# Performance work log

Measured on AMD Instinct MI355X. Metric: run time of the kernel, lower is better.

## Reference

```python
import jax, jax.numpy as jnp
import numpy as np

B, T, H, DK, DV, HID, C = 2, 4096, 16, 128, 128, 2048, 64  # chunk size 64 (fla default)
EPS = 1e-5


def setup_inputs() -> dict:
    key = jax.random.key(0)
    ks = jax.random.split(key, 8)
    s = 0.02
    return dict(
        hidden_ab=jax.random.normal(ks[0], (B, T, HID), jnp.float32),
        hidden_g=jax.random.normal(ks[1], (B, T, HID), jnp.float32),
        q=jax.random.normal(ks[2], (B, T, H, DK), jnp.float32),
        k=jax.random.normal(ks[3], (B, T, H, DK), jnp.float32),
        v=jax.random.normal(ks[4], (B, T, H, DV), jnp.float32),
        Wb=jax.random.normal(ks[5], (HID, H), jnp.float32) * s,
        Wg=jax.random.normal(ks[6], (HID, H), jnp.float32) * s,
        o_norm_w=jnp.ones((DV,), jnp.float32),
        o_proj_w=jax.random.normal(ks[7], (H, DV, DK), jnp.float32) * s,
    )


def _l2norm(x):
    return x * jax.lax.rsqrt(jnp.sum(x * x, -1, keepdims=True) + 1e-6)


def reference(hidden_ab, hidden_g, q, k, v, Wb, Wg, o_norm_w, o_proj_w):
    # beta gate per head (training path: sigmoid(b_proj(hidden_ab)))
    beta = jax.nn.sigmoid(hidden_ab @ Wb)  # [B,T,H]
    # qk_norm == 'l2' -> l2 normalization inside the kernel, q scaled by dk^-0.5
    q = _l2norm(q)
    k = _l2norm(k)
    scale = DK ** -0.5
    N = T // C

    def toc(x, d):  # [B,T,H,d] -> [N,B,H,C,d]
        return x.reshape(B, N, C, H, d).transpose(1, 0, 3, 2, 4)

    qc = toc(q * scale, DK)
    kc = toc(k, DK)
    vc = toc(v, DV)
    bc = beta.reshape(B, N, C, H).transpose(1, 0, 3, 2)  # [N,B,H,C]

    k_beta = kc * bc[..., None]
    v_beta = vc * bc[..., None]

    # intra-chunk UT transform: Tm = (I + strict_lower(k_beta k^T))^{-1}
    Lm = jnp.tril(jnp.einsum('nbhik,nbhjk->nbhij', k_beta, kc), -1)  # [N,B,H,C,C]
    eye = jnp.eye(C, dtype=q.dtype)
    Tm = jax.scipy.linalg.solve_triangular(eye + Lm, jnp.broadcast_to(eye, Lm.shape), lower=True)
    u = Tm @ v_beta   # [N,B,H,C,DV]
    w = Tm @ k_beta   # [N,B,H,C,DK]
    attn = jnp.tril(jnp.einsum('nbhik,nbhjk->nbhij', qc, kc))  # causal intra-chunk scores

    def step(S, ins):  # S: [B,H,DK,DV] carried state
        qn, kn, an, un, wn = ins
        vi = un - wn @ S                                   # corrected values
        on = qn @ S + an @ vi                              # inter + intra chunk output
        S = S + jnp.einsum('bhck,bhcv->bhkv', kn, vi)      # state update
        return S, on

    S0 = jnp.zeros((B, H, DK, DV), q.dtype)
    _, o = jax.lax.scan(step, S0, (qc, kc, attn, u, w))    # o: [N,B,H,C,DV]
    o = o.transpose(1, 0, 3, 2, 4).reshape(B, T, H, DV)

    # FusedRMSNormSwishGate with per-head scalar gate broadcast over DV
    g = hidden_g @ Wg  # [B,T,H]
    o = o * jax.lax.rsqrt(jnp.mean(o * o, -1, keepdims=True) + EPS) * o_norm_w
    o = o * (g * jax.nn.sigmoid(g))[..., None]

    # GroupLinear: per-head DV -> head_dim projection, then flatten heads
    out = jnp.einsum('bthv,hvd->bthd', o, o_proj_w).reshape(B, T, H * DK)
    return out
```

## Files before the change

kernel.cpp:

```cpp
#include <hip/hip_runtime.h>
#include <hip/hip_bf16.h>

#define BB 2
#define TT 4096
#define HH 16
#define DKk 128
#define DVv 128
#define HIDD 2048
#define CC 64
#define NN 64
#define GGS 16
#define QSCALE 0.08838834764831845f

static __device__ __forceinline__ unsigned short f2bf(float f) {
  unsigned u = __float_as_uint(f);
  u += 0x7fffu + ((u >> 16) & 1u);
  return (unsigned short)(u >> 16);
}
static __device__ __forceinline__ float bf2f(unsigned short s) {
  return __uint_as_float(((unsigned)s) << 16);
}

static __device__ __forceinline__ void barrier_lds_only() {
  asm volatile("s_waitcnt lgkmcnt(0)\n\ts_barrier" ::: "memory");
}

typedef short bf8 __attribute__((ext_vector_type(8)));
typedef short bf4 __attribute__((ext_vector_type(4)));
typedef float f4 __attribute__((ext_vector_type(4)));

static __device__ __forceinline__ bf4 pack_bf4(float a, float b, float c, float d) {
  bf4 r;
  r[0] = (short)f2bf(a); r[1] = (short)f2bf(b);
  r[2] = (short)f2bf(c); r[3] = (short)f2bf(d);
  return r;
}

__global__ __launch_bounds__(256) void k0_wt(
    const float* __restrict__ Wb, const float* __restrict__ Wg,
    unsigned short* __restrict__ Wtb, unsigned short* __restrict__ Wtg) {
  int blk = blockIdx.x;
  const float* W = (blk < 8) ? Wb : Wg;
  unsigned short* Wt = (blk < 8) ? Wtb : Wtg;
  int k0 = (blk & 7) * 256;
  int tid = threadIdx.x;
  __shared__ unsigned short st[16][272];
  const float* p = W + (size_t)(k0 + tid) * HH;
#pragma unroll
  for (int h4 = 0; h4 < 4; h4++) {
    float4 x = *(const float4*)(p + h4 * 4);
    st[h4 * 4 + 0][tid] = f2bf(x.x);
    st[h4 * 4 + 1][tid] = f2bf(x.y);
    st[h4 * 4 + 2][tid] = f2bf(x.z);
    st[h4 * 4 + 3][tid] = f2bf(x.w);
  }
  __syncthreads();
  int h = tid >> 4, c = (tid & 15) << 4;
#pragma unroll
  for (int j = 0; j < 16; j++)
    Wt[(size_t)h * HIDD + k0 + c + j] = st[h][c + j];
}

__global__ __launch_bounds__(256) void k0p_pt(
    const float* __restrict__ opw, unsigned short* __restrict__ Ppt) {
  int h = blockIdx.x;
  int tid = threadIdx.x;
  __shared__ unsigned short sp[128 * 132];
  const float* P = opw + (size_t)h * (DVv * DKk);
  for (int it = 0; it < 16; it++) {
    int idx = it * 256 + tid;
    int vv = idx >> 5, d4 = (idx & 31) << 2;
    float4 x = *(const float4*)(P + vv * 128 + d4);
    sp[vv * 132 + d4 + 0] = f2bf(x.x);
    sp[vv * 132 + d4 + 1] = f2bf(x.y);
    sp[vv * 132 + d4 + 2] = f2bf(x.z);
    sp[vv * 132 + d4 + 3] = f2bf(x.w);
  }
  __syncthreads();
  unsigned short* dst = Ppt + (size_t)h * (DVv * DKk);
  for (int it = 0; it < 8; it++) {
    int idx = it * 256 + tid;
    int d = idx >> 4, v8 = (idx & 15) << 3;
    unsigned short tmp[8];
#pragma unroll
    for (int j = 0; j < 8; j++) tmp[j] = sp[(v8 + j) * 132 + d];
    *(uint4*)&dst[d * 128 + v8] = *(uint4*)tmp;
  }
}

__global__ __launch_bounds__(256) void k1_beta_g(
    const float* __restrict__ hab, const float* __restrict__ hg,
    const unsigned short* __restrict__ Wtb, const unsigned short* __restrict__ Wtg,
    float* __restrict__ beta, float* __restrict__ graw) {
  int tile = blockIdx.x;
  int tid = threadIdx.x;
  int w = tid >> 6, lane = tid & 63;
  int proj = w >> 1, ks = w & 1;
  int n16 = lane & 15, qd = lane >> 4;
  const float* hid = proj ? hg : hab;
  const unsigned short* Wt = proj ? Wtg : Wtb;
  size_t rowbase = (size_t)(tile * 16 + n16) * HIDD;
  int k0 = ks * 1024;

  f4 acc = {0.f, 0.f, 0.f, 0.f};
  for (int s = 0; s < 32; s++) {
    int kk = k0 + s * 32 + qd * 8;
    const float* hp = hid + rowbase + kk;
    float4 h0 = *(const float4*)hp;
    float4 h1 = *(const float4*)(hp + 4);
    bf8 a;
    a[0] = (short)f2bf(h0.x); a[1] = (short)f2bf(h0.y);
    a[2] = (short)f2bf(h0.z); a[3] = (short)f2bf(h0.w);
    a[4] = (short)f2bf(h1.x); a[5] = (short)f2bf(h1.y);
    a[6] = (short)f2bf(h1.z); a[7] = (short)f2bf(h1.w);
    bf8 b = *(const bf8*)&Wt[(size_t)n16 * HIDD + kk];
    acc = __builtin_amdgcn_mfma_f32_16x16x32_bf16(a, b, acc, 0, 0, 0);
  }

  __shared__ float red[2][16][17];
  if (ks == 1) {
#pragma unroll
    for (int r = 0; r < 4; r++) red[proj][qd * 4 + r][n16] = acc[r];
  }
  __syncthreads();
  if (ks == 0) {
#pragma unroll
    for (int r = 0; r < 4; r++) {
      float s = acc[r] + red[proj][qd * 4 + r][n16];
      size_t t = (size_t)(tile * 16 + qd * 4 + r) * HH + n16;
      if (proj == 0) beta[t] = 1.f / (1.f + expf(-s));
      else           graw[t] = s;
    }
  }
}

__global__ __launch_bounds__(256) void k2_l2norm(
    const float* __restrict__ q, const float* __restrict__ k,
    unsigned short* __restrict__ qn, unsigned short* __restrict__ kn) {
  int lane = threadIdx.x & 63, wave = threadIdx.x >> 6;
  for (int u = 0; u < 2; u++) {
    int vec = blockIdx.x * 8 + wave * 2 + u;
    size_t off = (size_t)vec * 64 + lane;
    float2 q2 = ((const float2*)q)[off];
    float2 k2 = ((const float2*)k)[off];
    float sq = q2.x * q2.x + q2.y * q2.y;
    float sk = k2.x * k2.x + k2.y * k2.y;
#pragma unroll
    for (int m = 32; m; m >>= 1) { sq += __shfl_xor(sq, m); sk += __shfl_xor(sk, m); }
    float rq = rsqrtf(sq + 1e-6f) * QSCALE;
    float rk = rsqrtf(sk + 1e-6f);
    unsigned pq = (unsigned)f2bf(q2.x * rq) | ((unsigned)f2bf(q2.y * rq) << 16);
    unsigned pk = (unsigned)f2bf(k2.x * rk) | ((unsigned)f2bf(k2.y * rk) << 16);
    ((unsigned*)qn)[off] = pq;
    ((unsigned*)kn)[off] = pk;
  }
}

#define SW 72
#define K3_M0R 8704
#define K3_M0T 13312
#define K3_M1R 17920
#define K3_M1T 22528
#define K3_TB  27136
#define K3_ARENA 31744

__global__ __launch_bounds__(256) void k3_chunk(
    const unsigned short* __restrict__ qn, const unsigned short* __restrict__ kn,
    const float* __restrict__ beta,
    unsigned short* __restrict__ ATg, unsigned short* __restrict__ Ktg) {
  int cid = blockIdx.x;
  int n = cid & (NN - 1);
  int bh = cid / NN;
  int h = bh & (HH - 1);
  int b = bh / HH;
  int tid = threadIdx.x;
  int w = tid >> 6;
  int lane = tid & 63;
  int n16 = lane & 15;
  int qd = lane >> 4;
  int r0 = w * 16;

  __shared__ __align__(16) unsigned short arena[K3_ARENA];
  __shared__ float sb[CC];
  unsigned short* sk = arena;
  unsigned short* sq = arena + 8704;

  int t0 = n * CC;
#pragma unroll
  for (int p = 0; p < 4; p++) {
    int id = p * 256 + tid, row = id >> 4, c8 = (id & 15) << 3;
    size_t g = ((size_t)((b * TT + t0 + row) * HH + h)) * DKk + c8;
    *(uint4*)&sk[row * 136 + c8] = *(const uint4*)(kn + g);
    *(uint4*)&sq[row * 136 + c8] = *(const uint4*)(qn + g);
  }
  if (tid < CC) sb[tid] = beta[(size_t)((b * TT + t0 + tid) * HH + h)];
  __syncthreads();

  f4 at[4], mk[4];
#pragma unroll
  for (int ct = 0; ct < 4; ct++) { at[ct] = (f4){0,0,0,0}; mk[ct] = (f4){0,0,0,0}; }
#pragma unroll
  for (int s = 0; s < 4; s++) {
    bf8 aq = *(const bf8*)&sq[(r0 + n16) * 136 + s * 32 + qd * 8];
    bf8 ak = *(const bf8*)&sk[(r0 + n16) * 136 + s * 32 + qd * 8];
#pragma unroll
    for (int ct = 0; ct < 4; ct++) {
      bf8 bk = *(const bf8*)&sk[(ct * 16 + n16) * 136 + s * 32 + qd * 8];
      at[ct] = __builtin_amdgcn_mfma_f32_16x16x32_bf16(aq, bk, at[ct], 0, 0, 0);
      mk[ct] = __builtin_amdgcn_mfma_f32_16x16x32_bf16(ak, bk, mk[ct], 0, 0, 0);
    }
  }

  f4 tf[4];
  float mpv[4][4];
#pragma unroll
  for (int ct = 0; ct < 4; ct++) {
#pragma unroll
    for (int r = 0; r < 4; r++) {
      int i = r0 + qd * 4 + r, j = ct * 16 + n16;
      at[ct][r] = (j <= i) ? at[ct][r] : 0.f;
      float mp = (j < i) ? -sb[i] * mk[ct][r] : 0.f;
      mpv[ct][r] = mp;
      tf[ct][r] = (i == j) ? 1.f : mp;
    }
  }
  __syncthreads();

#pragma unroll
  for (int ct = 0; ct < 4; ct++) {
#pragma unroll
    for (int r = 0; r < 4; r++) {
      int i = r0 + qd * 4 + r, j = ct * 16 + n16;
      unsigned short hm = f2bf(mpv[ct][r]);
      arena[K3_M0R + i * SW + j] = hm;
      arena[K3_M0T + j * SW + i] = hm;
      arena[K3_TB + j * SW + i] = f2bf(tf[ct][r]);
    }
  }
  __syncthreads();

  int p = 0;
  for (int it = 1; it <= 5; it++) {
    int mrp = p ? K3_M1R : K3_M0R, mtp = p ? K3_M1T : K3_M0T;
    int mrn = p ? K3_M0R : K3_M1R, mtn = p ? K3_M0T : K3_M1T;
    f4 nr[4];
#pragma unroll
    for (int ct = 0; ct < 4; ct++) nr[ct] = (f4){0,0,0,0};
#pragma unroll
    for (int s = 0; s < 2; s++) {
      bf8 a = *(const bf8*)&arena[mrp + (r0 + n16) * SW + s * 32 + qd * 8];
#pragma unroll
      for (int ct = 0; ct < 4; ct++) {
        bf8 bb = *(const bf8*)&arena[mtp + (ct * 16 + n16) * SW + s * 32 + qd * 8];
        nr[ct] = __builtin_amdgcn_mfma_f32_16x16x32_bf16(a, bb, nr[ct], 0, 0, 0);
      }
    }
#pragma unroll
    for (int ct = 0; ct < 4; ct++) {
#pragma unroll
      for (int r = 0; r < 4; r++) {
        int i = r0 + qd * 4 + r, j = ct * 16 + n16;
        unsigned short hm = f2bf(nr[ct][r]);
        arena[mrn + i * SW + j] = hm;
        arena[mtn + j * SW + i] = hm;
      }
    }
    __syncthreads();

#pragma unroll
    for (int s = 0; s < 2; s++) {
      bf8 a = *(const bf8*)&arena[mrn + (r0 + n16) * SW + s * 32 + qd * 8];
#pragma unroll
      for (int ct = 0; ct < 4; ct++) {
        bf8 bb = *(const bf8*)&arena[K3_TB + (ct * 16 + n16) * SW + s * 32 + qd * 8];
        tf[ct] = __builtin_amdgcn_mfma_f32_16x16x32_bf16(a, bb, tf[ct], 0, 0, 0);
      }
    }
    __syncthreads();

    if (it < 5) {
#pragma unroll
      for (int ct = 0; ct < 4; ct++) {
#pragma unroll
        for (int r = 0; r < 4; r++) {
          int i = r0 + qd * 4 + r, j = ct * 16 + n16;
          arena[K3_TB + j * SW + i] = f2bf(tf[ct][r]);
        }
      }
    }
    p = 1 - p;
  }

#pragma unroll
  for (int ct = 0; ct < 4; ct++) {
#pragma unroll
    for (int r = 0; r < 4; r++) {
      int i = r0 + qd * 4 + r, j = ct * 16 + n16;
      arena[K3_M0R + i * SW + j] = f2bf(at[ct][r]);
      arena[K3_TB + j * SW + i] = f2bf(tf[ct][r]);
    }
  }
  __syncthreads();

  {
    f4 ac[4];
#pragma unroll
    for (int ct = 0; ct < 4; ct++) ac[ct] = (f4){0,0,0,0};
#pragma unroll
    for (int s = 0; s < 2; s++) {
      bf8 a = *(const bf8*)&arena[K3_M0R + (r0 + n16) * SW + s * 32 + qd * 8];
#pragma unroll
      for (int ct = 0; ct < 4; ct++) {
        bf8 bb = *(const bf8*)&arena[K3_TB + (ct * 16 + n16) * SW + s * 32 + qd * 8];
        ac[ct] = __builtin_amdgcn_mfma_f32_16x16x32_bf16(a, bb, ac[ct], 0, 0, 0);
      }
    }
    size_t abase = (size_t)cid * (CC * CC);
#pragma unroll
    for (int ct = 0; ct < 4; ct++)
#pragma unroll
      for (int r = 0; r < 4; r++)
        ATg[abase + (r0 + qd * 4 + r) * CC + ct * 16 + n16] = f2bf(ac[ct][r]);
  }

  {
    size_t kbase = (size_t)cid * (DKk * CC);
#pragma unroll
    for (int t = 0; t < 2; t++) {
      int dkt = w * 32 + t * 16;
      f4 ac[4];
#pragma unroll
      for (int ct = 0; ct < 4; ct++) ac[ct] = (f4){0,0,0,0};
#pragma unroll
      for (int s = 0; s < 2; s++) {
        bf8 a;
#pragma unroll
        for (int jj = 0; jj < 8; jj++)
          a[jj] = (short)sk[(s * 32 + qd * 8 + jj) * 136 + dkt + n16];
#pragma unroll
        for (int ct = 0; ct < 4; ct++) {
          bf8 bb = *(const bf8*)&arena[K3_TB + (ct * 16 + n16) * SW + s * 32 + qd * 8];
          ac[ct] = __builtin_amdgcn_mfma_f32_16x16x32_bf16(a, bb, ac[ct], 0, 0, 0);
        }
      }
#pragma unroll
      for (int ct = 0; ct < 4; ct++)
#pragma unroll
        for (int r = 0; r < 4; r++)
          Ktg[kbase + (dkt + qd * 4 + r) * CC + ct * 16 + n16] = f2bf(ac[ct][r]);
    }
  }
}

struct K4Frag {
  bf8 k0, k1, k2, k3;
  bf8 q0, q1, q2, q3;
  bf8 a0, a1;
  bf8 t0, t1, t2, t3;
  float4 vv;
  float b0, b1, b2, b3;
};

static __device__ __forceinline__ void k4_prefetch(
    K4Frag& F, int n,
    const unsigned short* knb, const unsigned short* qnb,
    const unsigned short* atb, const unsigned short* ktb,
    const float* vb, const float* bb) {
  const unsigned short* kp = knb + (size_t)n * (CC * HH * DKk);
  F.k0 = *(const bf8*)(kp);
  F.k1 = *(const bf8*)(kp + 32);
  F.k2 = *(const bf8*)(kp + 64);
  F.k3 = *(const bf8*)(kp + 96);
  const unsigned short* qp = qnb + (size_t)n * (CC * HH * DKk);
  F.q0 = *(const bf8*)(qp);
  F.q1 = *(const bf8*)(qp + 32);
  F.q2 = *(const bf8*)(qp + 64);
  F.q3 = *(const bf8*)(qp + 96);
  const unsigned short* ap = atb + (size_t)n * (CC * CC);
  F.a0 = *(const bf8*)(ap);
  F.a1 = *(const bf8*)(ap + 32);
  const unsigned short* tp = ktb + (size_t)n * (DKk * CC);
  F.t0 = *(const bf8*)(tp);
  F.t1 = *(const bf8*)(tp + 32);
  F.t2 = *(const bf8*)(tp + 1024);
  F.t3 = *(const bf8*)(tp + 1024 + 32);
  F.vv = *(const float4*)(vb + (size_t)n * (CC * HH * DVv));
  const float* bp = bb + (size_t)n * (CC * HH);
  F.b0 = bp[0]; F.b1 = bp[HH]; F.b2 = bp[2 * HH]; F.b3 = bp[3 * HH];
}

static __device__ __forceinline__ void k4_body(
    const K4Frag& F, K4Frag& FN, int n, bool pf, bool ostore,
    f4& S0, f4& S1,
    unsigned short* xT, unsigned short* sSb,
    float* opn,
    int n16, int qd, int r0, int dkbase,
    const unsigned short* knb, const unsigned short* qnb,
    const unsigned short* atb, const unsigned short* ktb,
    const float* vb, const float* bb) {
  if (pf) k4_prefetch(FN, n + 1, knb, qnb, atb, ktb, vb, bb);

  {
    int col = r0 + n16;
    xT[(qd * 4 + 0) * SW + col] = f2bf(F.vv.x);
    xT[(qd * 4 + 1) * SW + col] = f2bf(F.vv.y);
    xT[(qd * 4 + 2) * SW + col] = f2bf(F.vv.z);
    xT[(qd * 4 + 3) * SW + col] = f2bf(F.vv.w);
  }
  barrier_lds_only();

  f4 oacc;
  {
    bf8 bS0 = *(const bf8*)&sSb[n16 * 136 + 0 + qd * 8];
    bf8 bS1 = *(const bf8*)&sSb[n16 * 136 + 32 + qd * 8];
    bf8 bS2 = *(const bf8*)&sSb[n16 * 136 + 64 + qd * 8];
    bf8 bS3 = *(const bf8*)&sSb[n16 * 136 + 96 + qd * 8];
    f4 xa = {0.f, 0.f, 0.f, 0.f}, xc = {0.f, 0.f, 0.f, 0.f};
    f4 oa = {0.f, 0.f, 0.f, 0.f}, ob = {0.f, 0.f, 0.f, 0.f};
    xa = __builtin_amdgcn_mfma_f32_16x16x32_bf16(F.k0, bS0, xa, 0, 0, 0);
    xa = __builtin_amdgcn_mfma_f32_16x16x32_bf16(F.k1, bS1, xa, 0, 0, 0);
    xc = __builtin_amdgcn_mfma_f32_16x16x32_bf16(F.k2, bS2, xc, 0, 0, 0);
    xc = __builtin_amdgcn_mfma_f32_16x16x32_bf16(F.k3, bS3, xc, 0, 0, 0);
    oa = __builtin_amdgcn_mfma_f32_16x16x32_bf16(F.q0, bS0, oa, 0, 0, 0);
    oa = __builtin_amdgcn_mfma_f32_16x16x32_bf16(F.q1, bS1, oa, 0, 0, 0);
    ob = __builtin_amdgcn_mfma_f32_16x16x32_bf16(F.q2, bS2, ob, 0, 0, 0);
    ob = __builtin_amdgcn_mfma_f32_16x16x32_bf16(F.q3, bS3, ob, 0, 0, 0);
    oacc = oa + ob;
    bf4 vv4 = *(const bf4*)&xT[n16 * SW + r0 + qd * 4];
    float bv[4] = {F.b0, F.b1, F.b2, F.b3};
    float xr[4];
#pragma unroll
    for (int r = 0; r < 4; r++)
      xr[r] = bv[r] * (bf2f((unsigned short)vv4[r]) - (xa[r] + xc[r]));
    *(bf4*)&xT[n16 * SW + r0 + qd * 4] = pack_bf4(xr[0], xr[1], xr[2], xr[3]);
  }
  barrier_lds_only();

  {
    bf8 bx0 = *(const bf8*)&xT[n16 * SW + qd * 8];
    bf8 bx1 = *(const bf8*)&xT[n16 * SW + 32 + qd * 8];
    oacc = __builtin_amdgcn_mfma_f32_16x16x32_bf16(F.a0, bx0, oacc, 0, 0, 0);
    oacc = __builtin_amdgcn_mfma_f32_16x16x32_bf16(F.a1, bx1, oacc, 0, 0, 0);
    if (ostore) {
#pragma unroll
      for (int r = 0; r < 4; r++) opn[r * (HH * DVv)] = oacc[r];
    }
    S0 = __builtin_amdgcn_mfma_f32_16x16x32_bf16(F.t0, bx0, S0, 0, 0, 0);
    S0 = __builtin_amdgcn_mfma_f32_16x16x32_bf16(F.t1, bx1, S0, 0, 0, 0);
    S1 = __builtin_amdgcn_mfma_f32_16x16x32_bf16(F.t2, bx0, S1, 0, 0, 0);
    S1 = __builtin_amdgcn_mfma_f32_16x16x32_bf16(F.t3, bx1, S1, 0, 0, 0);
    *(bf4*)&sSb[n16 * 136 + dkbase + qd * 4] = pack_bf4(S0[0], S0[1], S0[2], S0[3]);
    *(bf4*)&sSb[n16 * 136 + dkbase + 16 + qd * 4] = pack_bf4(S1[0], S1[1], S1[2], S1[3]);
  }
}

__global__ __launch_bounds__(256, 2) void k4_scan(
    const unsigned short* __restrict__ qn, const unsigned short* __restrict__ kn,
    const float* __restrict__ v, const float* __restrict__ beta,
    const unsigned short* __restrict__ ATg, const unsigned short* __restrict__ Ktg,
    float* __restrict__ o) {
  int bi = blockIdx.x;
  int jg = bi >> 5;
  int bh = bi & 31;
  int h = bh & (HH - 1);
  int b = bh >> 4;
  int tid = threadIdx.x;
  int j0w = jg * 8;
  int jw = (jg == 15) ? 112 : jg * 8;
  int lo = j0w - jw;
  int w = tid >> 6;
  int lane = tid & 63;
  int n16 = lane & 15;
  int qd = lane >> 4;
  int r0 = w * 16;
  int dkbase = w * 32;
  bool ostore = ((unsigned)(n16 - lo)) < 8u;

  __shared__ __align__(16) unsigned short sSb[16 * 136];
  __shared__ __align__(16) unsigned short sxT[2][16 * SW];

  f4 S0 = {0.f, 0.f, 0.f, 0.f}, S1 = {0.f, 0.f, 0.f, 0.f};
  for (int i = tid; i < 16 * 136; i += 256) sSb[i] = 0;

  const unsigned short* knb =
      kn + ((size_t)((b * TT + r0 + n16) * HH + h)) * DKk + qd * 8;
  const unsigned short* qnb =
      qn + ((size_t)((b * TT + r0 + n16) * HH + h)) * DKk + qd * 8;
  size_t bhN = (size_t)(b * HH + h) * NN;
  const unsigned short* atb = ATg + bhN * (CC * CC) + (r0 + n16) * 64 + qd * 8;
  const unsigned short* ktb = Ktg + bhN * (DKk * CC) + (dkbase + n16) * 64 + qd * 8;
  const float* vb =
      v + ((size_t)((b * TT + r0 + n16) * HH + h)) * DVv + jw + qd * 4;
  const float* bb = beta + (size_t)((b * TT + r0 + qd * 4) * HH + h);
  float* opb =
      o + ((size_t)((b * TT + r0 + qd * 4) * HH + h)) * DVv + jw + n16;

  K4Frag FA, FB;
  k4_prefetch(FA, 0, knb, qnb, atb, ktb, vb, bb);

  for (int n = 0; n < NN; n += 2) {
    k4_body(FA, FB, n, true, ostore, S0, S1, sxT[0], sSb,
            opb + (size_t)n * (CC * HH * DVv),
            n16, qd, r0, dkbase, knb, qnb, atb, ktb, vb, bb);
    k4_body(FB, FA, n + 1, n + 2 < NN, ostore, S0, S1, sxT[1], sSb,
            opb + (size_t)(n + 1) * (CC * HH * DVv),
            n16, qd, r0, dkbase, knb, qnb, atb, ktb, vb, bb);
  }
}

__global__ __launch_bounds__(256) void k5_out(
    const float* __restrict__ graw, const float* __restrict__ onw,
    const unsigned short* __restrict__ Ppt, float* __restrict__ out) {
  int bi = blockIdx.x;
  int h = bi & (HH - 1);
  int tt = (bi >> 4) & 127;
  int b = bi >> 11;
  int t0 = tt * 32;
  int tid = threadIdx.x;
  int w = tid >> 6;
  int lane = tid & 63;
  int n16 = lane & 15;
  int qd = lane >> 4;

  __shared__ __align__(16) float so[32 * 132];
  __shared__ float smul[32];
  __shared__ float snw[DVv];

  for (int r = 0; r < 16; r++) {
    int idx = r * 256 + tid;
    int t = idx >> 7, d = idx & 127;
    so[t * 132 + d] = out[((size_t)((b * TT + t0 + t) * HH + h)) * DVv + d];
  }
  if (tid < DVv) snw[tid] = onw[tid];
  __syncthreads();

  {
    int t = tid >> 3, l8 = tid & 7;
    float ss = 0.f;
    for (int j = 0; j < 16; j++) { float x = so[t * 132 + l8 + (j << 3)]; ss += x * x; }
    ss += __shfl_down(ss, 4, 8);
    ss += __shfl_down(ss, 2, 8);
    ss += __shfl_down(ss, 1, 8);
    if (l8 == 0) {
      float rms = rsqrtf(ss * (1.f / 128.f) + 1e-5f);
      float gv = graw[(size_t)((b * TT + t0 + t) * HH + h)];
      float sig = 1.f / (1.f + expf(-gv));
      smul[t] = rms * gv * sig;
    }
  }
  __syncthreads();
  for (int r = 0; r < 16; r++) {
    int idx = r * 256 + tid;
    int t = idx >> 7, d = idx & 127;
    so[t * 132 + d] *= smul[t] * snw[d];
  }
  __syncthreads();

  {
    const unsigned short* Pb = Ppt + (size_t)h * (DVv * DKk);
    int dt0 = w * 2;
#pragma unroll
    for (int m = 0; m < 2; m++) {
      bf8 A[4];
#pragma unroll
      for (int ks = 0; ks < 4; ks++) {
        const float* sp = &so[(m * 16 + n16) * 132 + ks * 32 + qd * 8];
        float4 f0 = *(const float4*)sp;
        float4 f1 = *(const float4*)(sp + 4);
        A[ks][0] = (short)f2bf(f0.x); A[ks][1] = (short)f2bf(f0.y);
        A[ks][2] = (short)f2bf(f0.z); A[ks][3] = (short)f2bf(f0.w);
        A[ks][4] = (short)f2bf(f1.x); A[ks][5] = (short)f2bf(f1.y);
        A[ks][6] = (short)f2bf(f1.z); A[ks][7] = (short)f2bf(f1.w);
      }
#pragma unroll
      for (int dti = 0; dti < 2; dti++) {
        int dt = dt0 + dti;
        f4 acc = {0.f, 0.f, 0.f, 0.f};
#pragma unroll
        for (int ks = 0; ks < 4; ks++) {
          bf8 Bf = *(const bf8*)(Pb + (dt * 16 + n16) * 128 + ks * 32 + qd * 8);
          acc = __builtin_amdgcn_mfma_f32_16x16x32_bf16(A[ks], Bf, acc, 0, 0, 0);
        }
#pragma unroll
        for (int r = 0; r < 4; r++) {
          size_t go = ((size_t)(b * TT + t0 + m * 16 + qd * 4 + r)) * (HH * DKk)
                      + h * DKk + dt * 16 + n16;
          out[go] = acc[r];
        }
      }
    }
  }
}

extern "C" void kernel_launch(void* const* d_in, const int* in_sizes, int n_in,
                              void* d_out, int out_size, void* d_ws, size_t ws_size,
                              hipStream_t stream) {
  (void)in_sizes; (void)n_in; (void)out_size; (void)ws_size;
  const float* hab = (const float*)d_in[0];
  const float* hg  = (const float*)d_in[1];
  const float* q   = (const float*)d_in[2];
  const float* k   = (const float*)d_in[3];
  const float* v   = (const float*)d_in[4];
  const float* Wb  = (const float*)d_in[5];
  const float* Wg  = (const float*)d_in[6];
  const float* onw = (const float*)d_in[7];
  const float* opw = (const float*)d_in[8];
  float* out = (float*)d_out;

  char* ws = (char*)d_ws;
  float* beta          = (float*)(ws);
  float* graw          = (float*)(ws + 524288);
  unsigned short* qn   = (unsigned short*)(ws + 1048576);
  unsigned short* kn   = (unsigned short*)(ws + 34603008);
  unsigned short* ATg  = (unsigned short*)(ws + 68157440);
  unsigned short* Ktg  = (unsigned short*)(ws + 84934656);
  unsigned short* Wtb  = (unsigned short*)(ws + 118489088);
  unsigned short* Wtg  = (unsigned short*)(ws + 118554624);
  unsigned short* Ppt  = (unsigned short*)(ws + 118620160);

  hipLaunchKernelGGL(k0_wt, dim3(16), dim3(256), 0, stream,
                     Wb, Wg, Wtb, Wtg);
  hipLaunchKernelGGL(k0p_pt, dim3(HH), dim3(256), 0, stream,
                     opw, Ppt);
  hipLaunchKernelGGL(k1_beta_g, dim3(TT * BB / 16), dim3(256), 0, stream,
                     hab, hg, Wtb, Wtg, beta, graw);
  hipLaunchKernelGGL(k2_l2norm, dim3(BB * TT * HH / 8), dim3(256), 0, stream,
                     q, k, qn, kn);
  hipLaunchKernelGGL(k3_chunk, dim3(BB * HH * NN), dim3(256), 0, stream,
                     qn, kn, beta, ATg, Ktg);
  hipLaunchKernelGGL(k4_scan, dim3(BB * HH * GGS), dim3(256), 0, stream,
                     qn, kn, v, beta, ATg, Ktg, out);
  hipLaunchKernelGGL(k5_out, dim3(BB * (TT / 32) * HH), dim3(256), 0, stream,
                     graw, onw, Ppt, out);
}
```

Baseline: 649.8 us.

## Split scan into state-chain and output wave groups with double-buffered state

The scan kernel now uses 512 threads split into two wave groups. One group runs the serial state recurrence (corrected values and state update) at raised priority. The other computes the chunk outputs one step behind, reading a double-buffered copy of the state from LDS. Each block now covers 16 value columns instead of 8, which halves the grid and removes the overlapping-column store masking. Beta is also written in a transposed per-head layout so it can be loaded as a float4. The aim is to take the output MFMAs off the critical recurrence path, at the cost of fewer blocks and lower occupancy.

```diff
diff --git a/kernel.cpp b/kernel.cpp
--- a/kernel.cpp
+++ b/kernel.cpp
@@ -9,7 +9,7 @@
 #define HIDD 2048
 #define CC 64
 #define NN 64
-#define GGS 16
+#define GG 8
 #define QSCALE 0.08838834764831845f
 
 static __device__ __forceinline__ unsigned short f2bf(float f) {
@@ -91,7 +91,8 @@
 __global__ __launch_bounds__(256) void k1_beta_g(
     const float* __restrict__ hab, const float* __restrict__ hg,
     const unsigned short* __restrict__ Wtb, const unsigned short* __restrict__ Wtg,
-    float* __restrict__ beta, float* __restrict__ graw) {
+    float* __restrict__ beta, float* __restrict__ graw,
+    float* __restrict__ bt) {
   int tile = blockIdx.x;
   int tid = threadIdx.x;
   int w = tid >> 6, lane = tid & 63;
@@ -127,9 +128,17 @@
 #pragma unroll
     for (int r = 0; r < 4; r++) {
       float s = acc[r] + red[proj][qd * 4 + r][n16];
-      size_t t = (size_t)(tile * 16 + qd * 4 + r) * HH + n16;
-      if (proj == 0) beta[t] = 1.f / (1.f + expf(-s));
-      else           graw[t] = s;
+      int tg = tile * 16 + qd * 4 + r;
+      size_t t = (size_t)tg * HH + n16;
+      if (proj == 0) {
+        float bv = 1.f / (1.f + expf(-s));
+        beta[t] = bv;
+        int bb = tg >> 12;
+        int ti = tg & (TT - 1);
+        bt[((size_t)(bb * HH + n16)) * TT + ti] = bv;
+      } else {
+        graw[t] = s;
+      }
     }
   }
 }
@@ -352,25 +361,34 @@
   }
 }
 
-struct K4Frag {
+struct K4F {
   bf8 k0, k1, k2, k3;
+  bf8 t0, t1, t2, t3;
+  float4 vv;
+  float4 bb;
   bf8 q0, q1, q2, q3;
   bf8 a0, a1;
-  bf8 t0, t1, t2, t3;
-  float4 vv;
-  float b0, b1, b2, b3;
 };
 
-static __device__ __forceinline__ void k4_prefetch(
-    K4Frag& F, int n,
-    const unsigned short* knb, const unsigned short* qnb,
-    const unsigned short* atb, const unsigned short* ktb,
-    const float* vb, const float* bb) {
+static __device__ __forceinline__ void k4_pref_chain(
+    K4F& F, int n, const unsigned short* knb, const unsigned short* ktb,
+    const float* vb, const float* btb) {
   const unsigned short* kp = knb + (size_t)n * (CC * HH * DKk);
   F.k0 = *(const bf8*)(kp);
   F.k1 = *(const bf8*)(kp + 32);
   F.k2 = *(const bf8*)(kp + 64);
   F.k3 = *(const bf8*)(kp + 96);
+  const unsigned short* tp = ktb + (size_t)n * (DKk * CC);
+  F.t0 = *(const bf8*)(tp);
+  F.t1 = *(const bf8*)(tp + 32);
+  F.t2 = *(const bf8*)(tp + 1024);
+  F.t3 = *(const bf8*)(tp + 1056);
+  F.vv = *(const float4*)(vb + (size_t)n * (CC * HH * DVv));
+  F.bb = *(const float4*)(btb + n * CC);
+}
+
+static __device__ __forceinline__ void k4_pref_o(
+    K4F& F, int n, const unsigned short* qnb, const unsigned short* atb) {
   const unsigned short* qp = qnb + (size_t)n * (CC * HH * DKk);
   F.q0 = *(const bf8*)(qp);
   F.q1 = *(const bf8*)(qp + 32);
@@ -379,84 +397,87 @@
   const unsigned short* ap = atb + (size_t)n * (CC * CC);
   F.a0 = *(const bf8*)(ap);
   F.a1 = *(const bf8*)(ap + 32);
-  const unsigned short* tp = ktb + (size_t)n * (DKk * CC);
-  F.t0 = *(const bf8*)(tp);
-  F.t1 = *(const bf8*)(tp + 32);
-  F.t2 = *(const bf8*)(tp + 1024);
-  F.t3 = *(const bf8*)(tp + 1024 + 32);
-  F.vv = *(const float4*)(vb + (size_t)n * (CC * HH * DVv));
-  const float* bp = bb + (size_t)n * (CC * HH);
-  F.b0 = bp[0]; F.b1 = bp[HH]; F.b2 = bp[2 * HH]; F.b3 = bp[3 * HH];
 }
 
 static __device__ __forceinline__ void k4_body(
-    const K4Frag& F, K4Frag& FN, int n, bool pf, bool ostore,
+    const K4F& Fc, K4F& Fn, int i, int grp, bool pfc, bool pfo, bool odo,
     f4& S0, f4& S1,
-    unsigned short* xT, unsigned short* sSb,
-    float* opn,
+    unsigned short* xTc, const unsigned short* xTo,
+    const unsigned short* sSrd_c, unsigned short* sSwr_c,
+    const unsigned short* sSrd_o,
+    float* opb,
     int n16, int qd, int r0, int dkbase,
-    const unsigned short* knb, const unsigned short* qnb,
-    const unsigned short* atb, const unsigned short* ktb,
-    const float* vb, const float* bb) {
-  if (pf) k4_prefetch(FN, n + 1, knb, qnb, atb, ktb, vb, bb);
-
-  {
+    const unsigned short* knb, const unsigned short* ktb,
+    const float* vb, const float* btb,
+    const unsigned short* qnb, const unsigned short* atb) {
+  if (grp == 0) {
     int col = r0 + n16;
-    xT[(qd * 4 + 0) * SW + col] = f2bf(F.vv.x);
-    xT[(qd * 4 + 1) * SW + col] = f2bf(F.vv.y);
-    xT[(qd * 4 + 2) * SW + col] = f2bf(F.vv.z);
-    xT[(qd * 4 + 3) * SW + col] = f2bf(F.vv.w);
+    xTc[(qd * 4 + 0) * SW + col] = f2bf(Fc.vv.x);
+    xTc[(qd * 4 + 1) * SW + col] = f2bf(Fc.vv.y);
+    xTc[(qd * 4 + 2) * SW + col] = f2bf(Fc.vv.z);
+    xTc[(qd * 4 + 3) * SW + col] = f2bf(Fc.vv.w);
   }
   barrier_lds_only();
 
-  f4 oacc;
-  {
-    bf8 bS0 = *(const bf8*)&sSb[n16 * 136 + 0 + qd * 8];
-    bf8 bS1 = *(const bf8*)&sSb[n16 * 136 + 32 + qd * 8];
-    bf8 bS2 = *(const bf8*)&sSb[n16 * 136 + 64 + qd * 8];
-    bf8 bS3 = *(const bf8*)&sSb[n16 * 136 + 96 + qd * 8];
+  if (grp == 0) {
+    if (pfc) k4_pref_chain(Fn, i + 1, knb, ktb, vb, btb);
+    bf8 bS0 = *(const bf8*)&sSrd_c[n16 * 136 + 0  + qd * 8];
+    bf8 bS1 = *(const bf8*)&sSrd_c[n16 * 136 + 32 + qd * 8];
+    bf8 bS2 = *(const bf8*)&sSrd_c[n16 * 136 + 64 + qd * 8];
+    bf8 bS3 = *(const bf8*)&sSrd_c[n16 * 136 + 96 + qd * 8];
     f4 xa = {0.f, 0.f, 0.f, 0.f}, xc = {0.f, 0.f, 0.f, 0.f};
-    f4 oa = {0.f, 0.f, 0.f, 0.f}, ob = {0.f, 0.f, 0.f, 0.f};
-    xa = __builtin_amdgcn_mfma_f32_16x16x32_bf16(F.k0, bS0, xa, 0, 0, 0);
-    xa = __builtin_amdgcn_mfma_f32_16x16x32_bf16(F.k1, bS1, xa, 0, 0, 0);
-    xc = __builtin_amdgcn_mfma_f32_16x16x32_bf16(F.k2, bS2, xc, 0, 0, 0);
-    xc = __builtin_amdgcn_mfma_f32_16x16x32_bf16(F.k3, bS3, xc, 0, 0, 0);
-    oa = __builtin_amdgcn_mfma_f32_16x16x32_bf16(F.q0, bS0, oa, 0, 0, 0);
-    oa = __builtin_amdgcn_mfma_f32_16x16x32_bf16(F.q1, bS1, oa, 0, 0, 0);
-    ob = __builtin_amdgcn_mfma_f32_16x16x32_bf16(F.q2, bS2, ob, 0, 0, 0);
-    ob = __builtin_amdgcn_mfma_f32_16x16x32_bf16(F.q3, bS3, ob, 0, 0, 0);
-    oacc = oa + ob;
-    bf4 vv4 = *(const bf4*)&xT[n16 * SW + r0 + qd * 4];
-    float bv[4] = {F.b0, F.b1, F.b2, F.b3};
+    xa = __builtin_amdgcn_mfma_f32_16x16x32_bf16(Fc.k0, bS0, xa, 0, 0, 0);
+    xa = __builtin_amdgcn_mfma_f32_16x16x32_bf16(Fc.k1, bS1, xa, 0, 0, 0);
+    xc = __builtin_amdgcn_mfma_f32_16x16x32_bf16(Fc.k2, bS2, xc, 0, 0, 0);
+    xc = __builtin_amdgcn_mfma_f32_16x16x32_bf16(Fc.k3, bS3, xc, 0, 0, 0);
+    bf4 vv4 = *(const bf4*)&xTc[n16 * SW + r0 + qd * 4];
     float xr[4];
-#pragma unroll
-    for (int r = 0; r < 4; r++)
-      xr[r] = bv[r] * (bf2f((unsigned short)vv4[r]) - (xa[r] + xc[r]));
-    *(bf4*)&xT[n16 * SW + r0 + qd * 4] = pack_bf4(xr[0], xr[1], xr[2], xr[3]);
+    xr[0] = Fc.bb.x * (bf2f((unsigned short)vv4[0]) - (xa[0] + xc[0]));
+    xr[1] = Fc.bb.y * (bf2f((unsigned short)vv4[1]) - (xa[1] + xc[1]));
+    xr[2] = Fc.bb.z * (bf2f((unsigned short)vv4[2]) - (xa[2] + xc[2]));
+    xr[3] = Fc.bb.w * (bf2f((unsigned short)vv4[3]) - (xa[3] + xc[3]));
+    *(bf4*)&xTc[n16 * SW + r0 + qd * 4] = pack_bf4(xr[0], xr[1], xr[2], xr[3]);
+  } else {
+    if (pfo) k4_pref_o(Fn, i, qnb, atb);
+    if (odo) {
+      bf8 oS0 = *(const bf8*)&sSrd_o[n16 * 136 + 0  + qd * 8];
+      bf8 oS1 = *(const bf8*)&sSrd_o[n16 * 136 + 32 + qd * 8];
+      bf8 oS2 = *(const bf8*)&sSrd_o[n16 * 136 + 64 + qd * 8];
+      bf8 oS3 = *(const bf8*)&sSrd_o[n16 * 136 + 96 + qd * 8];
+      bf8 bx0 = *(const bf8*)&xTo[n16 * SW + 0  + qd * 8];
+      bf8 bx1 = *(const bf8*)&xTo[n16 * SW + 32 + qd * 8];
+      f4 oa = {0.f, 0.f, 0.f, 0.f}, ob = {0.f, 0.f, 0.f, 0.f};
+      oa = __builtin_amdgcn_mfma_f32_16x16x32_bf16(Fc.q0, oS0, oa, 0, 0, 0);
+      oa = __builtin_amdgcn_mfma_f32_16x16x32_bf16(Fc.q1, oS1, oa, 0, 0, 0);
+      ob = __builtin_amdgcn_mfma_f32_16x16x32_bf16(Fc.q2, oS2, ob, 0, 0, 0);
+      ob = __builtin_amdgcn_mfma_f32_16x16x32_bf16(Fc.q3, oS3, ob, 0, 0, 0);
+      f4 oo = oa + ob;
+      oo = __builtin_amdgcn_mfma_f32_16x16x32_bf16(Fc.a0, bx0, oo, 0, 0, 0);
+      oo = __builtin_amdgcn_mfma_f32_16x16x32_bf16(Fc.a1, bx1, oo, 0, 0, 0);
+      float* opn = opb + (size_t)(i - 1) * (CC * HH * DVv);
+#pragma unroll
+      for (int r = 0; r < 4; r++) opn[r * (HH * DVv)] = oo[r];
+    }
   }
   barrier_lds_only();
 
-  {
-    bf8 bx0 = *(const bf8*)&xT[n16 * SW + qd * 8];
-    bf8 bx1 = *(const bf8*)&xT[n16 * SW + 32 + qd * 8];
-    oacc = __builtin_amdgcn_mfma_f32_16x16x32_bf16(F.a0, bx0, oacc, 0, 0, 0);
-    oacc = __builtin_amdgcn_mfma_f32_16x16x32_bf16(F.a1, bx1, oacc, 0, 0, 0);
-    if (ostore) {
-#pragma unroll
-      for (int r = 0; r < 4; r++) opn[r * (HH * DVv)] = oacc[r];
-    }
-    S0 = __builtin_amdgcn_mfma_f32_16x16x32_bf16(F.t0, bx0, S0, 0, 0, 0);
-    S0 = __builtin_amdgcn_mfma_f32_16x16x32_bf16(F.t1, bx1, S0, 0, 0, 0);
-    S1 = __builtin_amdgcn_mfma_f32_16x16x32_bf16(F.t2, bx0, S1, 0, 0, 0);
-    S1 = __builtin_amdgcn_mfma_f32_16x16x32_bf16(F.t3, bx1, S1, 0, 0, 0);
-    *(bf4*)&sSb[n16 * 136 + dkbase + qd * 4] = pack_bf4(S0[0], S0[1], S0[2], S0[3]);
-    *(bf4*)&sSb[n16 * 136 + dkbase + 16 + qd * 4] = pack_bf4(S1[0], S1[1], S1[2], S1[3]);
-  }
-}
-
-__global__ __launch_bounds__(256, 2) void k4_scan(
+  if (grp == 0) {
+    bf8 bx0 = *(const bf8*)&xTc[n16 * SW + 0  + qd * 8];
+    bf8 bx1 = *(const bf8*)&xTc[n16 * SW + 32 + qd * 8];
+    S0 = __builtin_amdgcn_mfma_f32_16x16x32_bf16(Fc.t0, bx0, S0, 0, 0, 0);
+    S0 = __builtin_amdgcn_mfma_f32_16x16x32_bf16(Fc.t1, bx1, S0, 0, 0, 0);
+    S1 = __builtin_amdgcn_mfma_f32_16x16x32_bf16(Fc.t2, bx0, S1, 0, 0, 0);
+    S1 = __builtin_amdgcn_mfma_f32_16x16x32_bf16(Fc.t3, bx1, S1, 0, 0, 0);
+    *(bf4*)&sSwr_c[n16 * 136 + dkbase + qd * 4] =
+        pack_bf4(S0[0], S0[1], S0[2], S0[3]);
+    *(bf4*)&sSwr_c[n16 * 136 + dkbase + 16 + qd * 4] =
+        pack_bf4(S1[0], S1[1], S1[2], S1[3]);
+  }
+}
+
+__global__ __launch_bounds__(512, 1) void k4_scan(
     const unsigned short* __restrict__ qn, const unsigned short* __restrict__ kn,
-    const float* __restrict__ v, const float* __restrict__ beta,
+    const float* __restrict__ v, const float* __restrict__ bt,
     const unsigned short* __restrict__ ATg, const unsigned short* __restrict__ Ktg,
     float* __restrict__ o) {
   int bi = blockIdx.x;
@@ -465,46 +486,67 @@
   int h = bh & (HH - 1);
   int b = bh >> 4;
   int tid = threadIdx.x;
-  int j0w = jg * 8;
-  int jw = (jg == 15) ? 112 : jg * 8;
-  int lo = j0w - jw;
+  int j0 = jg * 16;
   int w = tid >> 6;
+  int grp = w >> 2;
+  int wl = w & 3;
   int lane = tid & 63;
   int n16 = lane & 15;
   int qd = lane >> 4;
-  int r0 = w * 16;
-  int dkbase = w * 32;
-  bool ostore = ((unsigned)(n16 - lo)) < 8u;
-
-  __shared__ __align__(16) unsigned short sSb[16 * 136];
+  int r0 = wl * 16;
+  int dkbase = wl * 32;
+
+  __shared__ __align__(16) unsigned short sSb[2][16 * 136];
   __shared__ __align__(16) unsigned short sxT[2][16 * SW];
 
   f4 S0 = {0.f, 0.f, 0.f, 0.f}, S1 = {0.f, 0.f, 0.f, 0.f};
-  for (int i = tid; i < 16 * 136; i += 256) sSb[i] = 0;
-
+  for (int i2 = tid; i2 < 2 * 16 * 136; i2 += 512) ((unsigned short*)sSb)[i2] = 0;
+
+  size_t bhN = (size_t)(b * HH + h) * NN;
   const unsigned short* knb =
       kn + ((size_t)((b * TT + r0 + n16) * HH + h)) * DKk + qd * 8;
   const unsigned short* qnb =
       qn + ((size_t)((b * TT + r0 + n16) * HH + h)) * DKk + qd * 8;
-  size_t bhN = (size_t)(b * HH + h) * NN;
   const unsigned short* atb = ATg + bhN * (CC * CC) + (r0 + n16) * 64 + qd * 8;
   const unsigned short* ktb = Ktg + bhN * (DKk * CC) + (dkbase + n16) * 64 + qd * 8;
   const float* vb =
-      v + ((size_t)((b * TT + r0 + n16) * HH + h)) * DVv + jw + qd * 4;
-  const float* bb = beta + (size_t)((b * TT + r0 + qd * 4) * HH + h);
+      v + ((size_t)((b * TT + r0 + n16) * HH + h)) * DVv + j0 + qd * 4;
+  const float* btb = bt + (size_t)(b * HH + h) * TT + r0 + qd * 4;
   float* opb =
-      o + ((size_t)((b * TT + r0 + qd * 4) * HH + h)) * DVv + jw + n16;
-
-  K4Frag FA, FB;
-  k4_prefetch(FA, 0, knb, qnb, atb, ktb, vb, bb);
-
-  for (int n = 0; n < NN; n += 2) {
-    k4_body(FA, FB, n, true, ostore, S0, S1, sxT[0], sSb,
-            opb + (size_t)n * (CC * HH * DVv),
-            n16, qd, r0, dkbase, knb, qnb, atb, ktb, vb, bb);
-    k4_body(FB, FA, n + 1, n + 2 < NN, ostore, S0, S1, sxT[1], sSb,
-            opb + (size_t)(n + 1) * (CC * HH * DVv),
-            n16, qd, r0, dkbase, knb, qnb, atb, ktb, vb, bb);
+      o + ((size_t)((b * TT + r0 + qd * 4) * HH + h)) * DVv + j0 + n16;
+
+  K4F FA, FB;
+  if (grp == 0) {
+    k4_pref_chain(FA, 0, knb, ktb, vb, btb);
+    __builtin_amdgcn_s_setprio(1);
+  }
+
+  for (int i = 0; i < NN; i += 2) {
+    k4_body(FA, FB, i, grp, i + 1 < NN, true, i > 0, S0, S1,
+            sxT[0], sxT[1], sSb[1], sSb[0], sSb[0], opb,
+            n16, qd, r0, dkbase, knb, ktb, vb, btb, qnb, atb);
+    k4_body(FB, FA, i + 1, grp, i + 2 < NN, i + 1 < NN, true, S0, S1,
+            sxT[1], sxT[0], sSb[0], sSb[1], sSb[1], opb,
+            n16, qd, r0, dkbase, knb, ktb, vb, btb, qnb, atb);
+  }
+  if (grp == 1) {
+    bf8 oS0 = *(const bf8*)&sSb[0][n16 * 136 + 0  + qd * 8];
+    bf8 oS1 = *(const bf8*)&sSb[0][n16 * 136 + 32 + qd * 8];
+    bf8 oS2 = *(const bf8*)&sSb[0][n16 * 136 + 64 + qd * 8];
+    bf8 oS3 = *(const bf8*)&sSb[0][n16 * 136 + 96 + qd * 8];
+    bf8 bx0 = *(const bf8*)&sxT[1][n16 * SW + 0  + qd * 8];
+    bf8 bx1 = *(const bf8*)&sxT[1][n16 * SW + 32 + qd * 8];
+    f4 oa = {0.f, 0.f, 0.f, 0.f}, ob = {0.f, 0.f, 0.f, 0.f};
+    oa = __builtin_amdgcn_mfma_f32_16x16x32_bf16(FA.q0, oS0, oa, 0, 0, 0);
+    oa = __builtin_amdgcn_mfma_f32_16x16x32_bf16(FA.q1, oS1, oa, 0, 0, 0);
+    ob = __builtin_amdgcn_mfma_f32_16x16x32_bf16(FA.q2, oS2, ob, 0, 0, 0);
+    ob = __builtin_amdgcn_mfma_f32_16x16x32_bf16(FA.q3, oS3, ob, 0, 0, 0);
+    f4 oo = oa + ob;
+    oo = __builtin_amdgcn_mfma_f32_16x16x32_bf16(FA.a0, bx0, oo, 0, 0, 0);
+    oo = __builtin_amdgcn_mfma_f32_16x16x32_bf16(FA.a1, bx1, oo, 0, 0, 0);
+    float* opn = opb + (size_t)(NN - 1) * (CC * HH * DVv);
+#pragma unroll
+    for (int r = 0; r < 4; r++) opn[r * (HH * DVv)] = oo[r];
   }
 }
 
@@ -617,19 +659,20 @@
   unsigned short* Wtb  = (unsigned short*)(ws + 118489088);
   unsigned short* Wtg  = (unsigned short*)(ws + 118554624);
   unsigned short* Ppt  = (unsigned short*)(ws + 118620160);
+  float* bt            = (float*)(ws + 119144448);
 
   hipLaunchKernelGGL(k0_wt, dim3(16), dim3(256), 0, stream,
                      Wb, Wg, Wtb, Wtg);
   hipLaunchKernelGGL(k0p_pt, dim3(HH), dim3(256), 0, stream,
                      opw, Ppt);
   hipLaunchKernelGGL(k1_beta_g, dim3(TT * BB / 16), dim3(256), 0, stream,
-                     hab, hg, Wtb, Wtg, beta, graw);
+                     hab, hg, Wtb, Wtg, beta, graw, bt);
   hipLaunchKernelGGL(k2_l2norm, dim3(BB * TT * HH / 8), dim3(256), 0, stream,
                      q, k, qn, kn);
   hipLaunchKernelGGL(k3_chunk, dim3(BB * HH * NN), dim3(256), 0, stream,
                      qn, kn, beta, ATg, Ktg);
-  hipLaunchKernelGGL(k4_scan, dim3(BB * HH * GGS), dim3(256), 0, stream,
-                     qn, kn, v, beta, ATg, Ktg, out);
+  hipLaunchKernelGGL(k4_scan, dim3(BB * HH * GG), dim3(512), 0, stream,
+                     qn, kn, v, bt, ATg, Ktg, out);
   hipLaunchKernelGGL(k5_out, dim3(BB * (TT / 32) * HH), dim3(256), 0, stream,
                      graw, onw, Ppt, out);
 }
```

Measured after the change: 523.7 us. 1.24x faster.
